# Optimization experiments

Hardware: AMD Instinct MI355X
Metric: run time of the kernel (lower is better)

The kernel has to match this reference:

```python
import jax, jax.numpy as jnp
import numpy as np

B, T, C, H = 4, 2048, 1024, 16
D = C // H
EPS = 1e-5


def setup_inputs() -> dict:
    key = jax.random.key(0)
    ks = jax.random.split(key, 8)
    s = 0.02
    return {
        "hidden_states": jax.random.normal(ks[0], (B, T, C), jnp.float32),
        "w_attn": jax.random.normal(ks[1], (C, 3 * C), jnp.float32) * s,
        "b_attn": jnp.zeros((3 * C,), jnp.float32),
        "w_proj": jax.random.normal(ks[2], (C, C), jnp.float32) * s,
        "b_proj": jnp.zeros((C,), jnp.float32),
        "ln1_g": jnp.ones((C,), jnp.float32),
        "ln1_b": jnp.zeros((C,), jnp.float32),
        "ln2_g": jnp.ones((C,), jnp.float32),
        "ln2_b": jnp.zeros((C,), jnp.float32),
        "w_fc": jax.random.normal(ks[3], (C, 4 * C), jnp.float32) * s,
        "b_fc": jnp.zeros((4 * C,), jnp.float32),
        "w_fc2": jax.random.normal(ks[4], (4 * C, C), jnp.float32) * s,
        "b_fc2": jnp.zeros((C,), jnp.float32),
    }


def _layernorm(x, g, b):
    mu = jnp.mean(x, axis=-1, keepdims=True)
    var = jnp.mean(jnp.square(x - mu), axis=-1, keepdims=True)
    return (x - mu) * jax.lax.rsqrt(var + EPS) * g + b


def _attention(x, w_attn, b_attn, w_proj, b_proj):
    Bx, Tx, Cx = x.shape
    qkv = x @ w_attn + b_attn  # [B,T,3C]  (GCLinear transpose=True => x @ W)
    q, k, v = jnp.split(qkv, 3, axis=-1)
    # [B,T,C] -> [B,H,T,D]
    q = q.reshape(Bx, Tx, H, D).transpose(0, 2, 1, 3)
    k = k.reshape(Bx, Tx, H, D).transpose(0, 2, 1, 3)
    v = v.reshape(Bx, Tx, H, D).transpose(0, 2, 1, 3)
    att = jnp.einsum("bhqd,bhkd->bhqk", q, k) * (1.0 / np.sqrt(D))
    causal = jnp.tril(jnp.ones((Tx, Tx), bool))
    att = jnp.where(causal, att, -jnp.inf)
    att = jax.nn.softmax(att, axis=-1)
    y = jnp.einsum("bhqk,bhkd->bhqd", att, v)
    y = y.transpose(0, 2, 1, 3).reshape(Bx, Tx, Cx)
    return y @ w_proj + b_proj


def reference(hidden_states, w_attn, b_attn, w_proj, b_proj,
              ln1_g, ln1_b, ln2_g, ln2_b, w_fc, b_fc, w_fc2, b_fc2):
    x = hidden_states
    a = _attention(_layernorm(x, ln1_g, ln1_b), w_attn, b_attn, w_proj, b_proj)
    x = x + a
    h = _layernorm(x, ln2_g, ln2_b)
    h = jax.nn.gelu(h @ w_fc + b_fc, approximate=False)  # nn.GELU default = exact erf
    h = h @ w_fc2 + b_fc2
    return x + h
```

## Files before the change

### kernel.cpp

```cpp
#include <hip/hip_runtime.h>
#include <hip/hip_bf16.h>
#include <stdint.h>

typedef __bf16 bf16_t;
typedef __bf16 bf16x8 __attribute__((ext_vector_type(8)));
typedef __bf16 bf16x4 __attribute__((ext_vector_type(4)));
typedef float f32x4 __attribute__((ext_vector_type(4)));
typedef short short4v __attribute__((ext_vector_type(4)));

#define BDIM_B 4
#define TDIM 2048
#define CDIM 1024

__device__ __forceinline__ void gload16(const void* g, void* l) {
  using GP = const __attribute__((address_space(1))) char*;
  using LP = __attribute__((address_space(3))) char*;
  __builtin_amdgcn_global_load_lds((GP)(uintptr_t)g, (LP)(uint32_t)(uintptr_t)l, 16, 0, 0);
}

__global__ __launch_bounds__(256)
void transpose_cast(const float* __restrict__ W, bf16_t* __restrict__ Wt, int K, int N) {
  __shared__ float tile[32][33];
  const int tx = threadIdx.x & 31, ty = threadIdx.x >> 5;
  const int n0 = blockIdx.x * 32, k0 = blockIdx.y * 32;
#pragma unroll
  for (int j = 0; j < 32; j += 8)
    tile[ty + j][tx] = W[(size_t)(k0 + ty + j) * N + n0 + tx];
  __syncthreads();
#pragma unroll
  for (int j = 0; j < 32; j += 8)
    Wt[(size_t)(n0 + ty + j) * K + k0 + tx] = (bf16_t)tile[tx][ty + j];
}

__global__ __launch_bounds__(256)
void ln_kernel(const float* __restrict__ x, const float* __restrict__ g,
               const float* __restrict__ bta, bf16_t* __restrict__ out) {
  const size_t row = blockIdx.x;
  const int tid = threadIdx.x;
  const float4 v = ((const float4*)(x + row * CDIM))[tid];
  float s = v.x + v.y + v.z + v.w;
#pragma unroll
  for (int off = 1; off < 64; off <<= 1) s += __shfl_xor(s, off);
  __shared__ float r1[4], r2[4];
  const int wv = tid >> 6, lane = tid & 63;
  if (!lane) r1[wv] = s;
  __syncthreads();
  const float mu = (r1[0] + r1[1] + r1[2] + r1[3]) * (1.f / CDIM);
  const float dx = v.x - mu, dy = v.y - mu, dz = v.z - mu, dw = v.w - mu;
  float q = dx * dx + dy * dy + dz * dz + dw * dw;
#pragma unroll
  for (int off = 1; off < 64; off <<= 1) q += __shfl_xor(q, off);
  if (!lane) r2[wv] = q;
  __syncthreads();
  const float var = (r2[0] + r2[1] + r2[2] + r2[3]) * (1.f / CDIM);
  const float rs = rsqrtf(var + 1e-5f);
  const float4 gg = ((const float4*)g)[tid];
  const float4 bb = ((const float4*)bta)[tid];
  bf16x4 o;
  o[0] = (bf16_t)(dx * rs * gg.x + bb.x);
  o[1] = (bf16_t)(dy * rs * gg.y + bb.y);
  o[2] = (bf16_t)(dz * rs * gg.z + bb.z);
  o[3] = (bf16_t)(dw * rs * gg.w + bb.w);
  ((bf16x4*)(out + row * CDIM))[tid] = o;
}

enum { EPI_BF16 = 0, EPI_RESID = 1, EPI_GELU = 2 };

template <int EPI>
__global__ __launch_bounds__(512)
void gemm256(const bf16_t* __restrict__ A, const bf16_t* __restrict__ Bt,
             const float* __restrict__ bias, const float* __restrict__ resid,
             void* __restrict__ outv, int M, int N, int K) {
  __shared__ bf16_t sA[2][256 * 64];
  __shared__ bf16_t sB[2][256 * 64];
  const int tid = threadIdx.x;
  const int lane = tid & 63, wv = tid >> 6;
  const int wm = wv >> 2, wn = wv & 3;
  const int rin = lane & 15, quad = lane >> 4;

  const int nwg = gridDim.x * gridDim.y;
  const int bid = blockIdx.y * gridDim.x + blockIdx.x;
  const int swzb = (bid & 7) * (nwg >> 3) + (bid >> 3);
  const int bx = swzb % gridDim.x, by = swzb / gridDim.x;
  const int m0 = by * 256, n0 = bx * 256;

  const int c8 = (lane & 7) ^ ((lane >> 3) & 7);
  const int aRow = wm * 128 + (wv & 3) * 8 + (lane >> 3);
  const int bRow = wn * 64 + (wv >> 2) * 8 + (lane >> 3);
  const bf16_t* srcA = A + (size_t)(m0 + aRow) * K + c8 * 8;
  const bf16_t* srcB = Bt + (size_t)(n0 + bRow) * K + c8 * 8;
  const int dstA = (wm * 128 + (wv & 3) * 8) * 64;
  const int dstB = (wn * 64 + (wv >> 2) * 8) * 64;

#define STA(buf, r, kk) gload16(srcA + (size_t)(32 * (r)) * K + (kk), (buf) + dstA + 32 * (r) * 64)
#define STB(buf, r, kk) gload16(srcB + (size_t)(16 * (r)) * K + (kk), (buf) + dstB + 16 * (r) * 64)

  const int ck0 = (quad ^ (rin & 7)) * 8;
  const int ck1 = ((4 + quad) ^ (rin & 7)) * 8;
  const int aBase = (wm * 128 + rin) * 64;
  const int bBase = (wn * 64 + rin) * 64;

  f32x4 acc[8][4] = {};
  bf16x8 af[8][2], bfr[4][2];

#define RDA(mi) { af[mi][0] = *(const bf16x8*)(rA + aBase + (mi)*1024 + ck0); \
                  af[mi][1] = *(const bf16x8*)(rA + aBase + (mi)*1024 + ck1); }
#define RDB(ni) { bfr[ni][0] = *(const bf16x8*)(rB + bBase + (ni)*1024 + ck0); \
                  bfr[ni][1] = *(const bf16x8*)(rB + bBase + (ni)*1024 + ck1); }
#define MM(mi, ni) { acc[mi][ni] = __builtin_amdgcn_mfma_f32_16x16x32_bf16(af[mi][0], bfr[ni][0], acc[mi][ni], 0, 0, 0); \
                     acc[mi][ni] = __builtin_amdgcn_mfma_f32_16x16x32_bf16(af[mi][1], bfr[ni][1], acc[mi][ni], 0, 0, 0); }

  const int NT = K >> 6;

  {
    bf16_t* wA = sA[0];
    bf16_t* wB = sB[0];
    STA(wA, 0, 0); STB(wB, 0, 0); STB(wB, 1, 0);
    STA(wA, 1, 0); STB(wB, 2, 0); STB(wB, 3, 0);
    STA(wA, 2, 0);
    STA(wA, 3, 0);
  }

  for (int t = 0; t < NT; ++t) {
    const bf16_t* rA = sA[t & 1];
    const bf16_t* rB = sB[t & 1];
    bf16_t* wA = sA[(t & 1) ^ 1];
    bf16_t* wB = sB[(t & 1) ^ 1];
    const int kk = (t + 1 < NT ? t + 1 : t) * 64;

    asm volatile("s_waitcnt vmcnt(5)" ::: "memory");
    __builtin_amdgcn_s_barrier();
    __builtin_amdgcn_sched_barrier(0);
    RDA(0) RDA(1) RDB(0) RDB(1)
    STA(wA, 0, kk); STB(wB, 0, kk); STB(wB, 1, kk);
    __builtin_amdgcn_s_setprio(1);
    MM(0, 0) MM(0, 1) MM(1, 0) MM(1, 1)
    __builtin_amdgcn_s_setprio(0);
    __builtin_amdgcn_sched_barrier(0);

    asm volatile("s_waitcnt vmcnt(5)" ::: "memory");
    __builtin_amdgcn_s_barrier();
    __builtin_amdgcn_sched_barrier(0);
    RDA(2) RDA(3) RDB(2) RDB(3)
    STA(wA, 1, kk); STB(wB, 2, kk); STB(wB, 3, kk);
    __builtin_amdgcn_s_setprio(1);
    MM(0, 2) MM(0, 3) MM(1, 2) MM(1, 3) MM(2, 0) MM(2, 1) MM(3, 0) MM(3, 1)
    __builtin_amdgcn_s_setprio(0);
    __builtin_amdgcn_sched_barrier(0);

    asm volatile("s_waitcnt vmcnt(7)" ::: "memory");
    __builtin_amdgcn_s_barrier();
    __builtin_amdgcn_sched_barrier(0);
    RDA(4) RDA(5)
    STA(wA, 2, kk);
    __builtin_amdgcn_s_setprio(1);
    MM(2, 2) MM(2, 3) MM(3, 2) MM(3, 3) MM(4, 0) MM(4, 1) MM(5, 0) MM(5, 1)
    __builtin_amdgcn_s_setprio(0);
    __builtin_amdgcn_sched_barrier(0);

    asm volatile("s_waitcnt vmcnt(7)" ::: "memory");
    __builtin_amdgcn_s_barrier();
    __builtin_amdgcn_sched_barrier(0);
    RDA(6) RDA(7)
    STA(wA, 3, kk);
    __builtin_amdgcn_s_setprio(1);
    MM(4, 2) MM(4, 3) MM(5, 2) MM(5, 3) MM(6, 0) MM(6, 1) MM(7, 0) MM(7, 1)
    MM(6, 2) MM(6, 3) MM(7, 2) MM(7, 3)
    __builtin_amdgcn_s_setprio(0);
    __builtin_amdgcn_sched_barrier(0);
  }
  asm volatile("s_waitcnt vmcnt(0)" ::: "memory");

  const int rbase = m0 + wm * 128 + quad * 4;
  const int cbase = n0 + wn * 64 + rin;
#pragma unroll
  for (int mi = 0; mi < 8; ++mi)
#pragma unroll
    for (int ni = 0; ni < 4; ++ni)
#pragma unroll
      for (int r = 0; r < 4; ++r) {
        const int m = rbase + mi * 16 + r;
        const int n = cbase + ni * 16;
        float v = acc[mi][ni][r] + bias[n];
        if (EPI == EPI_RESID) v += resid[(size_t)m * N + n];
        if (EPI == EPI_GELU) v = 0.5f * v * (1.0f + erff(v * 0.7071067811865476f));
        if (EPI == EPI_RESID)
          ((float*)outv)[(size_t)m * N + n] = v;
        else
          ((bf16_t*)outv)[(size_t)m * N + n] = (bf16_t)v;
      }
#undef STA
#undef STB
#undef RDA
#undef RDB
#undef MM
}

__global__ __launch_bounds__(256)
void attn_kernel(const bf16_t* __restrict__ qkv, bf16_t* __restrict__ y) {
  const int h = blockIdx.y, b = blockIdx.z;
  const int tid = threadIdx.x, lane = tid & 63, wv = tid >> 6;
  const int rin = lane & 15, quad = lane >> 4;

  __shared__ bf16_t Kt[64 * 64];
  __shared__ bf16_t Vt[64 * 64];

  const size_t base3 = (size_t)(b * TDIM) * 3072;
  const int srow = tid >> 2, sseg = tid & 3;
  const short4v ones = {(short)0x3F80, (short)0x3F80, (short)0x3F80, (short)0x3F80};

#pragma unroll 1
  for (int seg = 0; seg < 2; ++seg) {
    const int qt = seg ? blockIdx.x : (15 - blockIdx.x);
    const int q0 = qt * 128;
    const int nkt = qt * 2 + 2;

    bf16x8 aq[2][2];
#pragma unroll
    for (int qf = 0; qf < 2; ++qf) {
      const size_t qr = base3 + (size_t)(q0 + wv * 32 + qf * 16 + rin) * 3072 + h * 64;
#pragma unroll
      for (int ki = 0; ki < 2; ++ki)
        aq[qf][ki] = *(const bf16x8*)(qkv + qr + ki * 32 + quad * 8);
    }

    uint4 kreg[2], vreg[2];
#pragma unroll
    for (int hf = 0; hf < 2; ++hf) {
      const size_t gb = base3 + (size_t)srow * 3072 + h * 64 + hf * 32 + sseg * 8;
      kreg[hf] = *(const uint4*)(qkv + gb + 1024);
      vreg[hf] = *(const uint4*)(qkv + gb + 2048);
    }

    f32x4 o[2][4] = {};
    f32x4 ol[2] = {};

    for (int kt = 0; kt < nkt; ++kt) {
      __syncthreads();
      {
        const int krot = (srow >> 2) & 7;
        const int tg = srow >> 3, to = srow & 7;
#pragma unroll
        for (int hf = 0; hf < 2; ++hf) {
          const int g = hf * 4 + sseg;
          *(uint4*)(Kt + srow * 64 + (((g + krot) & 7) * 8)) = kreg[hf];
          union { uint4 u; bf16_t e[8]; } vv;
          vv.u = vreg[hf];
#pragma unroll
          for (int j = 0; j < 8; ++j) {
            const int d = hf * 32 + sseg * 8 + j;
            Vt[d * 64 + (((tg + ((d >> 2) & 7)) & 7) * 8) + to] = vv.e[j];
          }
        }
      }
      __syncthreads();
      {
        const int ktn = (kt + 1 < nkt) ? kt + 1 : kt;
#pragma unroll
        for (int hf = 0; hf < 2; ++hf) {
          const size_t gb = base3 + (size_t)(ktn * 64 + srow) * 3072 + h * 64 + hf * 32 + sseg * 8;
          kreg[hf] = *(const uint4*)(qkv + gb + 1024);
          vreg[hf] = *(const uint4*)(qkv + gb + 2048);
        }
      }
      f32x4 st[2][4] = {};
#pragma unroll
      for (int ki = 0; ki < 2; ++ki) {
        bf16x8 ak[4];
#pragma unroll
        for (int kf = 0; kf < 4; ++kf) {
          const int tr = kf * 16 + rin;
          ak[kf] = *(const bf16x8*)(Kt + tr * 64 + (((ki * 4 + quad + ((tr >> 2) & 7)) & 7) * 8));
        }
#pragma unroll
        for (int qf = 0; qf < 2; ++qf)
#pragma unroll
          for (int kf = 0; kf < 4; ++kf)
            st[qf][kf] = __builtin_amdgcn_mfma_f32_16x16x32_bf16(ak[kf], aq[qf][ki], st[qf][kf], 0, 0, 0);
      }
      const bool maskt = (kt >= 2 * qt);
      short4v pf[2][4];
#pragma unroll
      for (int qf = 0; qf < 2; ++qf) {
        const int qg = q0 + wv * 32 + qf * 16 + rin;
#pragma unroll
        for (int kf = 0; kf < 4; ++kf)
#pragma unroll
          for (int r = 0; r < 4; ++r) {
            const int kg = kt * 64 + kf * 16 + quad * 4 + r;
            float p = __builtin_amdgcn_exp2f(st[qf][kf][r] * 0.18033688f);
            if (maskt && kg > qg) p = 0.f;
            union { bf16_t bv; short sv; } cv;
            cv.bv = (bf16_t)p;
            pf[qf][kf][r] = cv.sv;
          }
      }
#pragma unroll
      for (int kf = 0; kf < 4; ++kf) {
        short4v bv[4];
#pragma unroll
        for (int nd = 0; nd < 4; ++nd) {
          const int d = nd * 16 + rin;
          const int sw = (2 * kf + (quad >> 1) + ((d >> 2) & 7)) & 7;
          bv[nd] = *(const short4v*)(Vt + d * 64 + sw * 8 + (quad & 1) * 4);
        }
#pragma unroll
        for (int qf = 0; qf < 2; ++qf) {
#pragma unroll
          for (int nd = 0; nd < 4; ++nd)
            o[qf][nd] = __builtin_amdgcn_mfma_f32_16x16x16bf16_1k(pf[qf][kf], bv[nd], o[qf][nd], 0, 0, 0);
          ol[qf] = __builtin_amdgcn_mfma_f32_16x16x16bf16_1k(pf[qf][kf], ones, ol[qf], 0, 0, 0);
        }
      }
    }

#pragma unroll
    for (int qf = 0; qf < 2; ++qf)
#pragma unroll
      for (int r = 0; r < 4; ++r) {
        const float inv = 1.0f / ol[qf][r];
        const size_t row = (size_t)b * TDIM + q0 + wv * 32 + qf * 16 + quad * 4 + r;
#pragma unroll
        for (int nd = 0; nd < 4; ++nd)
          y[row * CDIM + h * 64 + nd * 16 + rin] = (bf16_t)(o[qf][nd][r] * inv);
      }
  }
}

extern "C" void kernel_launch(void* const* d_in, const int* in_sizes, int n_in,
                              void* d_out, int out_size, void* d_ws, size_t ws_size,
                              hipStream_t stream) {
  const float* x      = (const float*)d_in[0];
  const float* w_attn = (const float*)d_in[1];
  const float* b_attn = (const float*)d_in[2];
  const float* w_proj = (const float*)d_in[3];
  const float* b_proj = (const float*)d_in[4];
  const float* ln1g   = (const float*)d_in[5];
  const float* ln1b   = (const float*)d_in[6];
  const float* ln2g   = (const float*)d_in[7];
  const float* ln2b   = (const float*)d_in[8];
  const float* w_fc   = (const float*)d_in[9];
  const float* b_fc   = (const float*)d_in[10];
  const float* w_fc2  = (const float*)d_in[11];
  const float* b_fc2  = (const float*)d_in[12];
  float* out = (float*)d_out;

  char* ws = (char*)d_ws;
  bf16_t* wTattn = (bf16_t*)(ws + 0);
  bf16_t* wTproj = (bf16_t*)(ws + 6291456);
  bf16_t* wTfc   = (bf16_t*)(ws + 8388608);
  bf16_t* wTfc2  = (bf16_t*)(ws + 16777216);
  bf16_t* xn     = (bf16_t*)(ws + 25165824);
  float*  x2     = (float*)(ws + 41943040);
  bf16_t* qkv    = (bf16_t*)(ws + 75497472);
  bf16_t* yb     = (bf16_t*)(ws + 75497472 + 50331648);
  bf16_t* hb     = (bf16_t*)(ws + 75497472);

  transpose_cast<<<dim3(96, 32), 256, 0, stream>>>(w_attn, wTattn, 1024, 3072);
  transpose_cast<<<dim3(32, 32), 256, 0, stream>>>(w_proj, wTproj, 1024, 1024);
  transpose_cast<<<dim3(128, 32), 256, 0, stream>>>(w_fc, wTfc, 1024, 4096);
  transpose_cast<<<dim3(32, 128), 256, 0, stream>>>(w_fc2, wTfc2, 4096, 1024);

  ln_kernel<<<8192, 256, 0, stream>>>(x, ln1g, ln1b, xn);
  gemm256<EPI_BF16><<<dim3(12, 32), 512, 0, stream>>>(xn, wTattn, b_attn, nullptr, qkv, 8192, 3072, 1024);
  attn_kernel<<<dim3(8, 16, 4), 256, 0, stream>>>(qkv, yb);
  gemm256<EPI_RESID><<<dim3(4, 32), 512, 0, stream>>>(yb, wTproj, b_proj, x, x2, 8192, 1024, 1024);
  ln_kernel<<<8192, 256, 0, stream>>>(x2, ln2g, ln2b, xn);
  gemm256<EPI_GELU><<<dim3(16, 32), 512, 0, stream>>>(xn, wTfc, b_fc, nullptr, hb, 8192, 4096, 1024);
  gemm256<EPI_RESID><<<dim3(4, 32), 512, 0, stream>>>(hb, wTfc2, b_fc2, x2, out, 8192, 1024, 4096);
}
```

Measured before the change: 550.2 us.

## Add 256x128 triple-buffered GEMM for narrow GEMMs and relax barrier waits

Adds a gemm128 kernel with a 256x128 tile and a three-stage LDS ring buffer that prefetches two K-steps ahead. It is used for the QKV, proj and fc2 GEMMs so the small-N GEMMs launch more workgroups and fill the GPU better. The existing gemm256 loop is also rescheduled: LDS fragment reads now come before the waitcnt/barrier, the sched_barriers are removed and the vmcnt thresholds are changed. In exchange, each tile reuses less data from LDS. The finer vmcnt accounting also risks hazards if the outstanding-load counts are wrong.

```diff
diff --git a/kernel.cpp b/kernel.cpp
--- a/kernel.cpp
+++ b/kernel.cpp
@@ -17,6 +17,8 @@
   using LP = __attribute__((address_space(3))) char*;
   __builtin_amdgcn_global_load_lds((GP)(uintptr_t)g, (LP)(uint32_t)(uintptr_t)l, 16, 0, 0);
 }
+
+#define S_BARRIER() asm volatile("s_barrier" ::: "memory")
 
 __global__ __launch_bounds__(256)
 void transpose_cast(const float* __restrict__ W, bf16_t* __restrict__ Wt, int K, int N) {
@@ -112,14 +114,12 @@
 
   const int NT = K >> 6;
 
-  {
-    bf16_t* wA = sA[0];
-    bf16_t* wB = sB[0];
-    STA(wA, 0, 0); STB(wB, 0, 0); STB(wB, 1, 0);
-    STA(wA, 1, 0); STB(wB, 2, 0); STB(wB, 3, 0);
-    STA(wA, 2, 0);
-    STA(wA, 3, 0);
-  }
+  STA(sA[0], 0, 0); STB(sB[0], 0, 0); STB(sB[0], 1, 0);
+  STA(sA[0], 1, 0); STB(sB[0], 2, 0); STB(sB[0], 3, 0);
+  STA(sA[0], 2, 0);
+  STA(sA[0], 3, 0);
+  asm volatile("s_waitcnt vmcnt(5)" ::: "memory");
+  S_BARRIER();
 
   for (int t = 0; t < NT; ++t) {
     const bf16_t* rA = sA[t & 1];
@@ -128,46 +128,38 @@
     bf16_t* wB = sB[(t & 1) ^ 1];
     const int kk = (t + 1 < NT ? t + 1 : t) * 64;
 
-    asm volatile("s_waitcnt vmcnt(5)" ::: "memory");
-    __builtin_amdgcn_s_barrier();
-    __builtin_amdgcn_sched_barrier(0);
     RDA(0) RDA(1) RDB(0) RDB(1)
+    asm volatile("s_waitcnt vmcnt(2)" ::: "memory");
+    S_BARRIER();
     STA(wA, 0, kk); STB(wB, 0, kk); STB(wB, 1, kk);
     __builtin_amdgcn_s_setprio(1);
     MM(0, 0) MM(0, 1) MM(1, 0) MM(1, 1)
     __builtin_amdgcn_s_setprio(0);
-    __builtin_amdgcn_sched_barrier(0);
-
-    asm volatile("s_waitcnt vmcnt(5)" ::: "memory");
-    __builtin_amdgcn_s_barrier();
-    __builtin_amdgcn_sched_barrier(0);
+
     RDA(2) RDA(3) RDB(2) RDB(3)
+    asm volatile("s_waitcnt vmcnt(4)" ::: "memory");
+    S_BARRIER();
     STA(wA, 1, kk); STB(wB, 2, kk); STB(wB, 3, kk);
     __builtin_amdgcn_s_setprio(1);
     MM(0, 2) MM(0, 3) MM(1, 2) MM(1, 3) MM(2, 0) MM(2, 1) MM(3, 0) MM(3, 1)
     __builtin_amdgcn_s_setprio(0);
-    __builtin_amdgcn_sched_barrier(0);
-
-    asm volatile("s_waitcnt vmcnt(7)" ::: "memory");
-    __builtin_amdgcn_s_barrier();
-    __builtin_amdgcn_sched_barrier(0);
+
     RDA(4) RDA(5)
+    asm volatile("s_waitcnt vmcnt(6)" ::: "memory");
+    S_BARRIER();
     STA(wA, 2, kk);
     __builtin_amdgcn_s_setprio(1);
     MM(2, 2) MM(2, 3) MM(3, 2) MM(3, 3) MM(4, 0) MM(4, 1) MM(5, 0) MM(5, 1)
     __builtin_amdgcn_s_setprio(0);
-    __builtin_amdgcn_sched_barrier(0);
-
-    asm volatile("s_waitcnt vmcnt(7)" ::: "memory");
-    __builtin_amdgcn_s_barrier();
-    __builtin_amdgcn_sched_barrier(0);
+
     RDA(6) RDA(7)
+    asm volatile("s_waitcnt vmcnt(4)" ::: "memory");
+    S_BARRIER();
     STA(wA, 3, kk);
     __builtin_amdgcn_s_setprio(1);
     MM(4, 2) MM(4, 3) MM(5, 2) MM(5, 3) MM(6, 0) MM(6, 1) MM(7, 0) MM(7, 1)
     MM(6, 2) MM(6, 3) MM(7, 2) MM(7, 3)
     __builtin_amdgcn_s_setprio(0);
-    __builtin_amdgcn_sched_barrier(0);
   }
   asm volatile("s_waitcnt vmcnt(0)" ::: "memory");
 
@@ -175,6 +167,111 @@
   const int cbase = n0 + wn * 64 + rin;
 #pragma unroll
   for (int mi = 0; mi < 8; ++mi)
+#pragma unroll
+    for (int ni = 0; ni < 4; ++ni)
+#pragma unroll
+      for (int r = 0; r < 4; ++r) {
+        const int m = rbase + mi * 16 + r;
+        const int n = cbase + ni * 16;
+        float v = acc[mi][ni][r] + bias[n];
+        if (EPI == EPI_RESID) v += resid[(size_t)m * N + n];
+        if (EPI == EPI_GELU) v = 0.5f * v * (1.0f + erff(v * 0.7071067811865476f));
+        if (EPI == EPI_RESID)
+          ((float*)outv)[(size_t)m * N + n] = v;
+        else
+          ((bf16_t*)outv)[(size_t)m * N + n] = (bf16_t)v;
+      }
+#undef STA
+#undef STB
+#undef RDA
+#undef RDB
+#undef MM
+}
+
+template <int EPI>
+__global__ __launch_bounds__(512)
+void gemm128(const bf16_t* __restrict__ A, const bf16_t* __restrict__ Bt,
+             const float* __restrict__ bias, const float* __restrict__ resid,
+             void* __restrict__ outv, int M, int N, int K) {
+  __shared__ bf16_t sA[3][256 * 64];
+  __shared__ bf16_t sB[3][128 * 64];
+  const int tid = threadIdx.x;
+  const int lane = tid & 63, wv = tid >> 6;
+  const int wm = wv >> 1, wn = wv & 1;
+  const int rin = lane & 15, quad = lane >> 4;
+
+  const int nwg = gridDim.x * gridDim.y;
+  const int bid = blockIdx.y * gridDim.x + blockIdx.x;
+  const int swzb = (bid & 7) * (nwg >> 3) + (bid >> 3);
+  const int bx = swzb % gridDim.x, by = swzb / gridDim.x;
+  const int m0 = by * 256, n0 = bx * 128;
+
+  const int c8 = (lane & 7) ^ ((lane >> 3) & 7);
+  const bf16_t* srcA = A + (size_t)(m0 + 8 * wv + (lane >> 3)) * K + c8 * 8;
+  const int dstA = (8 * wv) * 64;
+  const bf16_t* srcB = Bt + (size_t)(n0 + (wv >> 2) * 64 + (wv & 3) * 8 + (lane >> 3)) * K + c8 * 8;
+  const int dstB = ((wv >> 2) * 64 + (wv & 3) * 8) * 64;
+
+#define STA(buf, r, kk) gload16(srcA + (size_t)(64 * (r)) * K + (kk), (buf) + dstA + 64 * (r) * 64)
+#define STB(buf, r, kk) gload16(srcB + (size_t)(32 * (r)) * K + (kk), (buf) + dstB + 32 * (r) * 64)
+
+  const int ck0 = (quad ^ (rin & 7)) * 8;
+  const int ck1 = ((4 + quad) ^ (rin & 7)) * 8;
+  const int aBase = (wm * 64 + rin) * 64;
+  const int bBase = (wn * 64 + rin) * 64;
+
+  f32x4 acc[4][4] = {};
+  bf16x8 af[4][2], bfr[4][2];
+
+#define RDA(mi) { af[mi][0] = *(const bf16x8*)(rA + aBase + (mi)*1024 + ck0); \
+                  af[mi][1] = *(const bf16x8*)(rA + aBase + (mi)*1024 + ck1); }
+#define RDB(ni) { bfr[ni][0] = *(const bf16x8*)(rB + bBase + (ni)*1024 + ck0); \
+                  bfr[ni][1] = *(const bf16x8*)(rB + bBase + (ni)*1024 + ck1); }
+#define MM(mi, ni) { acc[mi][ni] = __builtin_amdgcn_mfma_f32_16x16x32_bf16(af[mi][0], bfr[ni][0], acc[mi][ni], 0, 0, 0); \
+                     acc[mi][ni] = __builtin_amdgcn_mfma_f32_16x16x32_bf16(af[mi][1], bfr[ni][1], acc[mi][ni], 0, 0, 0); }
+
+  const int NT = K >> 6;
+
+  STA(sA[0], 0, 0); STA(sA[0], 1, 0); STA(sA[0], 2, 0); STA(sA[0], 3, 0); STB(sB[0], 0, 0);
+  STB(sB[0], 1, 0);
+  STA(sA[1], 0, 64); STA(sA[1], 1, 64); STA(sA[1], 2, 64); STA(sA[1], 3, 64); STB(sB[1], 0, 64);
+  STB(sB[1], 1, 64);
+  asm volatile("s_waitcnt vmcnt(7)" ::: "memory");
+  S_BARRIER();
+
+  int rb = 0, wb = 2;
+  for (int t = 0; t < NT; ++t) {
+    const bf16_t* rA = sA[rb];
+    const bf16_t* rB = sB[rb];
+    bf16_t* wA = sA[wb];
+    bf16_t* wB = sB[wb];
+    const int kk = (t + 2 < NT ? t + 2 : NT - 1) * 64;
+
+    RDA(0) RDA(1) RDA(2) RDA(3) RDB(0) RDB(1)
+    asm volatile("s_waitcnt vmcnt(6)" ::: "memory");
+    S_BARRIER();
+    STA(wA, 0, kk); STA(wA, 1, kk); STA(wA, 2, kk); STA(wA, 3, kk); STB(wB, 0, kk);
+    __builtin_amdgcn_s_setprio(1);
+    MM(0, 0) MM(0, 1) MM(1, 0) MM(1, 1) MM(2, 0) MM(2, 1) MM(3, 0) MM(3, 1)
+    __builtin_amdgcn_s_setprio(0);
+
+    RDB(2) RDB(3)
+    asm volatile("s_waitcnt vmcnt(6)" ::: "memory");
+    S_BARRIER();
+    STB(wB, 1, kk);
+    __builtin_amdgcn_s_setprio(1);
+    MM(0, 2) MM(0, 3) MM(1, 2) MM(1, 3) MM(2, 2) MM(2, 3) MM(3, 2) MM(3, 3)
+    __builtin_amdgcn_s_setprio(0);
+
+    rb = (rb == 2) ? 0 : rb + 1;
+    wb = (wb == 2) ? 0 : wb + 1;
+  }
+  asm volatile("s_waitcnt vmcnt(0)" ::: "memory");
+
+  const int rbase = m0 + wm * 64 + quad * 4;
+  const int cbase = n0 + wn * 64 + rin;
+#pragma unroll
+  for (int mi = 0; mi < 4; ++mi)
 #pragma unroll
     for (int ni = 0; ni < 4; ++ni)
 #pragma unroll
@@ -362,10 +459,10 @@
   transpose_cast<<<dim3(32, 128), 256, 0, stream>>>(w_fc2, wTfc2, 4096, 1024);
 
   ln_kernel<<<8192, 256, 0, stream>>>(x, ln1g, ln1b, xn);
-  gemm256<EPI_BF16><<<dim3(12, 32), 512, 0, stream>>>(xn, wTattn, b_attn, nullptr, qkv, 8192, 3072, 1024);
+  gemm128<EPI_BF16><<<dim3(24, 32), 512, 0, stream>>>(xn, wTattn, b_attn, nullptr, qkv, 8192, 3072, 1024);
   attn_kernel<<<dim3(8, 16, 4), 256, 0, stream>>>(qkv, yb);
-  gemm256<EPI_RESID><<<dim3(4, 32), 512, 0, stream>>>(yb, wTproj, b_proj, x, x2, 8192, 1024, 1024);
+  gemm128<EPI_RESID><<<dim3(8, 32), 512, 0, stream>>>(yb, wTproj, b_proj, x, x2, 8192, 1024, 1024);
   ln_kernel<<<8192, 256, 0, stream>>>(x2, ln2g, ln2b, xn);
   gemm256<EPI_GELU><<<dim3(16, 32), 512, 0, stream>>>(xn, wTfc, b_fc, nullptr, hb, 8192, 4096, 1024);
-  gemm256<EPI_RESID><<<dim3(4, 32), 512, 0, stream>>>(hb, wTfc2, b_fc2, x2, out, 8192, 1024, 4096);
-}
+  gemm128<EPI_RESID><<<dim3(8, 32), 512, 0, stream>>>(hb, wTfc2, b_fc2, x2, out, 8192, 1024, 4096);
+}
```

New measurement: 511.8 us. 7.0% less time.
